# Optimization experiments

Hardware: AMD Instinct MI355X
Metric: run time of the kernel (lower is better)

## Reference

```python
import jax, jax.numpy as jnp
import numpy as np


def setup_inputs() -> dict:
    key = jax.random.key(0)
    ks = jax.random.split(key, 7)
    B, Sq, St, E = 4, 2048, 2048, 512
    s = E ** -0.5
    return {
        "query": jax.random.normal(ks[0], (B, Sq, E), jnp.float32),
        "target": jax.random.normal(ks[1], (B, St, E), jnp.float32),
        "bias": jax.random.normal(ks[2], (1, 1, Sq, St), jnp.float32),
        "Wq": jax.random.normal(ks[3], (E, E), jnp.float32) * s,
        "Wk": jax.random.normal(ks[4], (E, E), jnp.float32) * s,
        "Wv": jax.random.normal(ks[5], (E, E), jnp.float32) * s,
        "Wo": jax.random.normal(ks[6], (E, E), jnp.float32) * s,
    }


def reference(query, target, bias, Wq, Wk, Wv, Wo):
    B, Sq, E = query.shape
    St = target.shape[1]
    H = 8
    hd = E // H  # head_size

    q = query @ Wq   # [B, Sq, E]
    k = target @ Wk  # [B, St, E]
    v = target @ Wv  # [B, St, E]

    # split heads: [B, S, E] -> [B, H, S, hd]
    q = q.reshape(B, Sq, H, hd).transpose(0, 2, 1, 3)
    k = k.reshape(B, St, H, hd).transpose(0, 2, 1, 3)
    v = v.reshape(B, St, H, hd).transpose(0, 2, 1, 3)

    # scores: [B, H, Sq, St]
    weight = jnp.einsum('bhqd,bhtd->bhqt', q, k) / jnp.sqrt(jnp.float32(hd))
    weight = weight + bias
    weight = jax.nn.softmax(weight, axis=-1)
    # dropout: inference mode (training=False) -> identity

    out = jnp.einsum('bhqt,bhtd->bhqd', weight, v)  # [B, H, Sq, hd]
    out = out.transpose(0, 2, 1, 3).reshape(B, Sq, E)  # merge heads
    return out @ Wo
```

## Files before the change

### kernel.cpp

```cpp
#include <hip/hip_runtime.h>
#include <cstdint>

#define B_ 4
#define SQ_ 2048
#define ST_ 2048
#define E_ 512
#define H_ 8
#define HD_ 64
#define LDQ_ (3 * E_)
#define QS_ 0.18033688011112043f
#define L2E_ 1.44269504089f
#define BC_ 14.0f

typedef _Float16 f16_t;
typedef _Float16 f16x8 __attribute__((ext_vector_type(8)));
typedef _Float16 f16x4 __attribute__((ext_vector_type(4)));
typedef float f32x4 __attribute__((ext_vector_type(4)));

static __device__ __forceinline__ f16x8 ld8(const f16_t* p) {
  return *reinterpret_cast<const f16x8*>(p);
}

static __device__ __forceinline__ float fast_exp2(float x) {
  float r;
  asm("v_exp_f32 %0, %1" : "=v"(r) : "v"(x));
  return r;
}

static __device__ __forceinline__ void gld16(const f16_t* g, f16_t* l) {
  __builtin_amdgcn_global_load_lds((const __attribute__((address_space(1))) void*)g,
                                   (__attribute__((address_space(3))) void*)l, 16, 0, 0);
}

static __device__ __forceinline__ int swz(int row, int ch) {
  return row * 64 + (((ch ^ (row & 7)) & 7) << 3);
}

__global__ __launch_bounds__(256) void preproc_kernel(const float* __restrict__ query,
                                                      const float* __restrict__ target,
                                                      const float* __restrict__ bias,
                                                      const float* __restrict__ Wq,
                                                      const float* __restrict__ Wk,
                                                      const float* __restrict__ Wv,
                                                      const float* __restrict__ Wo,
                                                      f16_t* __restrict__ qb,
                                                      f16_t* __restrict__ tb,
                                                      f16x4* __restrict__ biasRT,
                                                      f16_t* __restrict__ WqkvT,
                                                      f16_t* __restrict__ WoT) {
  __shared__ float smem[64 * 65];
  const int g = blockIdx.x;
  const int tid = threadIdx.x;
  if (g < 8192) {
    const int n4 = (B_ * SQ_ * E_) / 4;
    int i = g * 256 + tid;
    const float* in = query;
    f16_t* out = qb;
    if (i >= n4) { i -= n4; in = target; out = tb; }
    float4 v = reinterpret_cast<const float4*>(in)[i];
    f16x4 o = {(f16_t)v.x, (f16_t)v.y, (f16_t)v.z, (f16_t)v.w};
    reinterpret_cast<f16x4*>(out)[i] = o;
  } else if (g < 9216) {
    const int gb = g - 8192;
    const int t0 = (gb & 31) * 64;
    const int q0 = (gb >> 5) * 64;
    for (int i = tid; i < 64 * 64; i += 256) {
      const int q = i >> 6, t = i & 63;
      smem[q * 65 + t] = bias[(size_t)(q0 + q) * ST_ + t0 + t];
    }
    __syncthreads();
#pragma unroll
    for (int s = 0; s < 4; ++s) {
      const int slot = s * 256 + tid;
      const int tile_id = slot >> 6;
      const int lane = slot & 63;
      const int tq = tile_id >> 2, tt = tile_id & 3;
      const int quad = lane >> 4, l16 = lane & 15;
      f16x4 v;
#pragma unroll
      for (int r = 0; r < 4; ++r)
        v[r] = (f16_t)(smem[(tq * 16 + l16) * 65 + tt * 16 + quad * 4 + r] * L2E_ - BC_);
      const size_t qb16 = (q0 >> 4) + tq, tb16 = (t0 >> 4) + tt;
      biasRT[(qb16 * 128 + tb16) * 64 + lane] = v;
    }
  } else {
    const int gw = g - 9216;
    const int w = gw >> 8;
    const float* W = (w == 0) ? Wq : (w == 1) ? Wk : (w == 2) ? Wv : Wo;
    f16_t* Wt = (w < 3) ? WqkvT + (size_t)w * E_ * E_ : WoT;
    const float sc = (w == 0) ? QS_ : 1.0f;
    const int bx = (gw & 15) * 32;
    const int by = ((gw >> 4) & 15) * 32;
    const int tx = tid & 31;
    const int ty = tid >> 5;
#pragma unroll
    for (int i = 0; i < 4; ++i)
      smem[(ty + i * 8) * 33 + tx] = W[(size_t)(by + ty + i * 8) * E_ + bx + tx];
    __syncthreads();
#pragma unroll
    for (int i = 0; i < 4; ++i)
      Wt[(size_t)(bx + ty + i * 8) * E_ + by + tx] = (f16_t)(smem[tx * 33 + ty + i * 8] * sc);
  }
}

__global__ __launch_bounds__(256) void vtrans_kernel(const f16_t* __restrict__ Vsrc,
                                                     f16_t* __restrict__ VT) {
  __shared__ f16_t tile[64][72];
  const int bh = blockIdx.y;
  const int b = bh >> 3, h = bh & 7;
  const int t0 = blockIdx.x * 64;
  for (int i = threadIdx.x; i < 64 * 64; i += 256) {
    const int t = i >> 6, d = i & 63;
    tile[d][t] = Vsrc[(size_t)(b * ST_ + t0 + t) * LDQ_ + h * HD_ + d];
  }
  __syncthreads();
  for (int i = threadIdx.x; i < 64 * 64; i += 256) {
    const int d = i >> 6, t = i & 63;
    VT[(size_t)(bh * HD_ + d) * ST_ + t0 + t] = tile[d][t];
  }
}

template <bool OUT_F16>
__global__ __launch_bounds__(256) void gemm_bt2_kernel(const f16_t* __restrict__ Aq,
                                                       const f16_t* __restrict__ Akv,
                                                       const f16_t* __restrict__ Bt,
                                                       void* __restrict__ Cv,
                                                       int K, int ldc) {
  __shared__ f16_t As[128 * 32];
  __shared__ f16_t Bs[128 * 32];
  const int tid = threadIdx.x;
  const int lane = tid & 63;
  const int wave = tid >> 6;
  const int wm = (wave >> 1) * 64;
  const int wn = (wave & 1) * 64;
  const int m0 = blockIdx.y * 128;
  const int n0 = blockIdx.x * 128;
  const int l16 = lane & 15;
  const int quad = lane >> 4;
  const f16_t* A = (n0 < E_) ? Aq : Akv;

  f32x4 acc[4][4] = {};

  const int r0 = wave * 16 + (lane >> 2);
  const int r1 = (wave + 4) * 16 + (lane >> 2);
  const int c0 = (lane & 3) * 8;
  const f16_t* Ag0 = A + (size_t)(m0 + r0) * K + c0;
  const f16_t* Ag1 = A + (size_t)(m0 + r1) * K + c0;
  const f16_t* Bg0 = Bt + (size_t)(n0 + r0) * K + c0;
  const f16_t* Bg1 = Bt + (size_t)(n0 + r1) * K + c0;
  f16_t* Al0 = &As[wave * 512 + lane * 8];
  f16_t* Al1 = &As[(wave + 4) * 512 + lane * 8];
  f16_t* Bl0 = &Bs[wave * 512 + lane * 8];
  f16_t* Bl1 = &Bs[(wave + 4) * 512 + lane * 8];

  for (int k0 = 0; k0 < K; k0 += 32) {
    __syncthreads();
    gld16(Ag0 + k0, Al0);
    gld16(Ag1 + k0, Al1);
    gld16(Bg0 + k0, Bl0);
    gld16(Bg1 + k0, Bl1);
    __syncthreads();
    f16x8 af[4], bfr[4];
#pragma unroll
    for (int i = 0; i < 4; ++i) af[i] = ld8(&As[(wm + i * 16 + l16) * 32 + quad * 8]);
#pragma unroll
    for (int j = 0; j < 4; ++j) bfr[j] = ld8(&Bs[(wn + j * 16 + l16) * 32 + quad * 8]);
#pragma unroll
    for (int i = 0; i < 4; ++i)
#pragma unroll
      for (int j = 0; j < 4; ++j)
        acc[i][j] = __builtin_amdgcn_mfma_f32_16x16x32_f16(af[i], bfr[j], acc[i][j], 0, 0, 0);
  }

#pragma unroll
  for (int i = 0; i < 4; ++i)
#pragma unroll
    for (int r = 0; r < 4; ++r) {
      const size_t row = (size_t)m0 + wm + i * 16 + quad * 4 + r;
#pragma unroll
      for (int j = 0; j < 4; ++j) {
        const size_t col = (size_t)n0 + wn + j * 16 + l16;
        if (OUT_F16)
          reinterpret_cast<f16_t*>(Cv)[row * (size_t)ldc + col] = (f16_t)acc[i][j][r];
        else
          reinterpret_cast<float*>(Cv)[row * (size_t)ldc + col] = acc[i][j][r];
      }
    }
}

__global__ __launch_bounds__(256, 4) void attn_kernel(const f16_t* __restrict__ QKV,
                                                      const f16_t* __restrict__ VT,
                                                      const f16x4* __restrict__ biasRT,
                                                      f16_t* __restrict__ O) {
  __shared__ f16_t Ks[2][64 * 64];
  __shared__ f16_t Vs[2][64 * 64];
  __shared__ f16_t Ps[4][1024];
  const int id = blockIdx.x;
  const int bh = id & 31;
  const int b = bh >> 3, h = bh & 7;
  const int q0 = (id >> 5) * 64;
  const int tid = threadIdx.x;
  const int wave = tid >> 6;
  const int lane = tid & 63;
  const int l16 = lane & 15;
  const int quad = lane >> 4;
  const int qw = q0 + wave * 16;

  const f16_t* qptr = QKV + (size_t)(b * SQ_ + qw + l16) * LDQ_ + h * HD_ + quad * 8;
  const f16x8 bq0 = ld8(qptr);
  const f16x8 bq1 = ld8(qptr + 32);

  const int ch0 = wave * 2, ch1 = ch0 + 1;
  const int rsub = lane >> 3;
  const int csub = (((lane & 7) ^ (lane >> 3)) << 3);
  const f16_t* kg0 = QKV + (size_t)(b * ST_ + ch0 * 8 + rsub) * LDQ_ + E_ + h * HD_ + csub;
  const f16_t* kg1 = QKV + (size_t)(b * ST_ + ch1 * 8 + rsub) * LDQ_ + E_ + h * HD_ + csub;
  const f16_t* vg0 = VT + (size_t)(bh * HD_ + ch0 * 8 + rsub) * ST_ + csub;
  const f16_t* vg1 = VT + (size_t)(bh * HD_ + ch1 * 8 + rsub) * ST_ + csub;
  const int loff0 = ch0 * 512 + lane * 8;
  const int loff1 = ch1 * 512 + lane * 8;

  const f16x4* bRT = biasRT + (size_t)(qw >> 4) * 128 * 64 + lane;

  gld16(kg0, &Ks[0][loff0]);
  gld16(kg1, &Ks[0][loff1]);
  gld16(vg0, &Vs[0][loff0]);
  gld16(vg1, &Vs[0][loff1]);
  kg0 += 64 * LDQ_;
  kg1 += 64 * LDQ_;
  vg0 += 64;
  vg1 += 64;
  f16x4 nb[4];
#pragma unroll
  for (int tt = 0; tt < 4; ++tt) nb[tt] = bRT[(size_t)tt * 64];

  f32x4 facc[4] = {};
  f32x4 lacc = {};
  int cur = 0;
  __syncthreads();

  for (int t0 = 0; t0 < ST_; t0 += 64) {
    const int nxt = cur ^ 1;
    f16x4 nbn[4];
    if (t0 + 64 < ST_) {
      gld16(kg0, &Ks[nxt][loff0]);
      gld16(kg1, &Ks[nxt][loff1]);
      gld16(vg0, &Vs[nxt][loff0]);
      gld16(vg1, &Vs[nxt][loff1]);
      kg0 += 64 * LDQ_;
      kg1 += 64 * LDQ_;
      vg0 += 64;
      vg1 += 64;
      const f16x4* bn = bRT + (size_t)((t0 + 64) >> 4) * 64;
#pragma unroll
      for (int tt = 0; tt < 4; ++tt) nbn[tt] = bn[(size_t)tt * 64];
    }

    f32x4 s[4];
#pragma unroll
    for (int tt = 0; tt < 4; ++tt) {
      const int row = tt * 16 + l16;
      f32x4 a;
#pragma unroll
      for (int r = 0; r < 4; ++r) a[r] = (float)nb[tt][r];
      a = __builtin_amdgcn_mfma_f32_16x16x32_f16(ld8(&Ks[cur][swz(row, quad)]), bq0, a, 0, 0, 0);
      a = __builtin_amdgcn_mfma_f32_16x16x32_f16(ld8(&Ks[cur][swz(row, quad + 4)]), bq1, a, 0, 0, 0);
      s[tt] = a;
    }

    f16x4 pk[4];
#pragma unroll
    for (int tt = 0; tt < 4; ++tt) {
#pragma unroll
      for (int r = 0; r < 4; ++r) {
        const float pv = fast_exp2(s[tt][r]);
        lacc[r] += pv;
        pk[tt][r] = (f16_t)pv;
      }
    }

    __syncthreads();

    f16_t* psb = Ps[wave];
#pragma unroll
    for (int tt = 0; tt < 4; ++tt) {
      const int p = tt * 2 + (quad >> 1);
      *reinterpret_cast<f16x4*>(&psb[(p * 16 + l16) * 8 + (quad & 1) * 4]) = pk[tt];
    }

#pragma unroll
    for (int tc = 0; tc < 2; ++tc) {
      const f16x8 ap = ld8(&psb[((tc * 4 + quad) * 16 + l16) * 8]);
#pragma unroll
      for (int j = 0; j < 4; ++j) {
        const f16x8 bv = ld8(&Vs[cur][swz(j * 16 + l16, tc * 4 + quad)]);
        facc[j] = __builtin_amdgcn_mfma_f32_16x16x32_f16(ap, bv, facc[j], 0, 0, 0);
      }
    }

    __syncthreads();

    if (t0 + 64 < ST_) {
#pragma unroll
      for (int tt = 0; tt < 4; ++tt) nb[tt] = nbn[tt];
    }
    cur = nxt;
  }

  float l_i = lacc[0] + lacc[1] + lacc[2] + lacc[3];
  l_i += __shfl_xor(l_i, 16);
  l_i += __shfl_xor(l_i, 32);
#pragma unroll
  for (int r = 0; r < 4; ++r) {
    const float lr = __shfl(l_i, quad * 4 + r);
    const float inv = 1.0f / lr;
    f16_t* op = O + (size_t)(b * SQ_ + qw + quad * 4 + r) * E_ + h * HD_ + l16;
#pragma unroll
    for (int j = 0; j < 4; ++j) op[j * 16] = (f16_t)(facc[j][r] * inv);
  }
}

extern "C" void kernel_launch(void* const* d_in, const int* in_sizes, int n_in,
                              void* d_out, int out_size, void* d_ws, size_t ws_size,
                              hipStream_t stream) {
  (void)in_sizes; (void)n_in; (void)out_size; (void)ws_size;
  const float* query = (const float*)d_in[0];
  const float* target = (const float*)d_in[1];
  const float* bias = (const float*)d_in[2];
  const float* Wq = (const float*)d_in[3];
  const float* Wk = (const float*)d_in[4];
  const float* Wv = (const float*)d_in[5];
  const float* Wo = (const float*)d_in[6];

  char* ws = (char*)d_ws;
  const size_t ACT = (size_t)B_ * SQ_ * E_;
  const size_t ACT_B = ACT * sizeof(f16_t);
  const size_t BIAS_B = (size_t)SQ_ * ST_ * sizeof(f16_t);
  const size_t W_B = (size_t)E_ * E_ * sizeof(f16_t);

  f16_t* qb = (f16_t*)(ws);
  f16_t* tb = (f16_t*)(ws + ACT_B);
  f16_t* biasRT = (f16_t*)(ws + 2 * ACT_B);
  f16_t* WqkvT = (f16_t*)(ws + 2 * ACT_B + BIAS_B);
  f16_t* WoT = WqkvT + 3 * (size_t)E_ * E_;
  f16_t* QKV = (f16_t*)(ws + 2 * ACT_B + BIAS_B + 4 * W_B);
  f16_t* VT = qb;
  f16_t* attn = tb;

  dim3 blk(256);
  preproc_kernel<<<dim3(10240), blk, 0, stream>>>(query, target, bias, Wq, Wk, Wv, Wo, qb, tb,
                                                  (f16x4*)biasRT, WqkvT, WoT);

  gemm_bt2_kernel<true><<<dim3(3 * E_ / 128, B_ * SQ_ / 128), blk, 0, stream>>>(
      qb, tb, WqkvT, QKV, E_, LDQ_);

  vtrans_kernel<<<dim3(ST_ / 64, B_ * H_), blk, 0, stream>>>(QKV + 2 * E_, VT);

  attn_kernel<<<dim3(SQ_ / 64 * B_ * H_), blk, 0, stream>>>(QKV, VT, (const f16x4*)biasRT, attn);

  gemm_bt2_kernel<false><<<dim3(E_ / 128, B_ * SQ_ / 128), blk, 0, stream>>>(
      attn, attn, WoT, (void*)d_out, E_, E_);
}
```

Measured before the change: 213.1 us.

## Double-buffer GEMM LDS tiles and use narrower N tile for output projection

The GEMM kernel now double-buffers its shared-memory A/B tiles, issuing the next k-slice's global loads before computing the current one, so each iteration needs one barrier instead of two. The kernel is also templated on N tile width. The output projection uses a 128x64 tile, which doubles its block count to improve CU occupancy on a small N=512 problem. LDS use per block doubles, and the narrower tile reuses each A load less.

```diff
diff --git a/kernel.cpp b/kernel.cpp
--- a/kernel.cpp
+++ b/kernel.cpp
@@ -120,26 +120,27 @@
   }
 }
 
-template <bool OUT_F16>
+template <bool OUT_F16, int TN>
 __global__ __launch_bounds__(256) void gemm_bt2_kernel(const f16_t* __restrict__ Aq,
                                                        const f16_t* __restrict__ Akv,
                                                        const f16_t* __restrict__ Bt,
                                                        void* __restrict__ Cv,
                                                        int K, int ldc) {
-  __shared__ f16_t As[128 * 32];
-  __shared__ f16_t Bs[128 * 32];
+  constexpr int MI = (TN == 128) ? 4 : 2;
+  __shared__ f16_t As[2][128 * 32];
+  __shared__ f16_t Bs[2][TN * 32];
   const int tid = threadIdx.x;
   const int lane = tid & 63;
   const int wave = tid >> 6;
-  const int wm = (wave >> 1) * 64;
-  const int wn = (wave & 1) * 64;
+  const int wm = (TN == 128) ? (wave >> 1) * 64 : wave * 32;
+  const int wn = (TN == 128) ? (wave & 1) * 64 : 0;
   const int m0 = blockIdx.y * 128;
-  const int n0 = blockIdx.x * 128;
+  const int n0 = blockIdx.x * TN;
   const int l16 = lane & 15;
   const int quad = lane >> 4;
   const f16_t* A = (n0 < E_) ? Aq : Akv;
 
-  f32x4 acc[4][4] = {};
+  f32x4 acc[MI][4] = {};
 
   const int r0 = wave * 16 + (lane >> 2);
   const int r1 = (wave + 4) * 16 + (lane >> 2);
@@ -148,32 +149,41 @@
   const f16_t* Ag1 = A + (size_t)(m0 + r1) * K + c0;
   const f16_t* Bg0 = Bt + (size_t)(n0 + r0) * K + c0;
   const f16_t* Bg1 = Bt + (size_t)(n0 + r1) * K + c0;
-  f16_t* Al0 = &As[wave * 512 + lane * 8];
-  f16_t* Al1 = &As[(wave + 4) * 512 + lane * 8];
-  f16_t* Bl0 = &Bs[wave * 512 + lane * 8];
-  f16_t* Bl1 = &Bs[(wave + 4) * 512 + lane * 8];
+  const int aoff0 = wave * 512 + lane * 8;
+  const int aoff1 = (wave + 4) * 512 + lane * 8;
+
+  gld16(Ag0, &As[0][aoff0]);
+  gld16(Ag1, &As[0][aoff1]);
+  gld16(Bg0, &Bs[0][aoff0]);
+  if (TN == 128) gld16(Bg1, &Bs[0][aoff1]);
+  int cur = 0;
+  __syncthreads();
 
   for (int k0 = 0; k0 < K; k0 += 32) {
-    __syncthreads();
-    gld16(Ag0 + k0, Al0);
-    gld16(Ag1 + k0, Al1);
-    gld16(Bg0 + k0, Bl0);
-    gld16(Bg1 + k0, Bl1);
-    __syncthreads();
-    f16x8 af[4], bfr[4];
-#pragma unroll
-    for (int i = 0; i < 4; ++i) af[i] = ld8(&As[(wm + i * 16 + l16) * 32 + quad * 8]);
-#pragma unroll
-    for (int j = 0; j < 4; ++j) bfr[j] = ld8(&Bs[(wn + j * 16 + l16) * 32 + quad * 8]);
-#pragma unroll
-    for (int i = 0; i < 4; ++i)
+    const int nx = cur ^ 1;
+    const int kn = k0 + 32;
+    if (kn < K) {
+      gld16(Ag0 + kn, &As[nx][aoff0]);
+      gld16(Ag1 + kn, &As[nx][aoff1]);
+      gld16(Bg0 + kn, &Bs[nx][aoff0]);
+      if (TN == 128) gld16(Bg1 + kn, &Bs[nx][aoff1]);
+    }
+    f16x8 af[MI], bfr[4];
+#pragma unroll
+    for (int i = 0; i < MI; ++i) af[i] = ld8(&As[cur][(wm + i * 16 + l16) * 32 + quad * 8]);
+#pragma unroll
+    for (int j = 0; j < 4; ++j) bfr[j] = ld8(&Bs[cur][(wn + j * 16 + l16) * 32 + quad * 8]);
+#pragma unroll
+    for (int i = 0; i < MI; ++i)
 #pragma unroll
       for (int j = 0; j < 4; ++j)
         acc[i][j] = __builtin_amdgcn_mfma_f32_16x16x32_f16(af[i], bfr[j], acc[i][j], 0, 0, 0);
-  }
-
-#pragma unroll
-  for (int i = 0; i < 4; ++i)
+    __syncthreads();
+    cur = nx;
+  }
+
+#pragma unroll
+  for (int i = 0; i < MI; ++i)
 #pragma unroll
     for (int r = 0; r < 4; ++r) {
       const size_t row = (size_t)m0 + wm + i * 16 + quad * 4 + r;
@@ -351,13 +361,13 @@
   preproc_kernel<<<dim3(10240), blk, 0, stream>>>(query, target, bias, Wq, Wk, Wv, Wo, qb, tb,
                                                   (f16x4*)biasRT, WqkvT, WoT);
 
-  gemm_bt2_kernel<true><<<dim3(3 * E_ / 128, B_ * SQ_ / 128), blk, 0, stream>>>(
+  gemm_bt2_kernel<true, 128><<<dim3(3 * E_ / 128, B_ * SQ_ / 128), blk, 0, stream>>>(
       qb, tb, WqkvT, QKV, E_, LDQ_);
 
   vtrans_kernel<<<dim3(ST_ / 64, B_ * H_), blk, 0, stream>>>(QKV + 2 * E_, VT);
 
   attn_kernel<<<dim3(SQ_ / 64 * B_ * H_), blk, 0, stream>>>(QKV, VT, (const f16x4*)biasRT, attn);
 
-  gemm_bt2_kernel<false><<<dim3(E_ / 128, B_ * SQ_ / 128), blk, 0, stream>>>(
+  gemm_bt2_kernel<false, 64><<<dim3(E_ / 64, B_ * SQ_ / 128), blk, 0, stream>>>(
       attn, attn, WoT, (void*)d_out, E_, E_);
 }
```

Result: no change. 209.6 us (-1.6%).
